# Performance work log

Hardware: AMD Instinct MI355X
Metric: run time of the kernel (lower is better)

Reference implementation:

```python
import jax, jax.numpy as jnp
import numpy as np

N_NODES = 100000
N_EDGES = 3200000
N_GRAPHS = 128
F_IN, HID = 16, 64


def setup_inputs() -> dict:
    key = jax.random.key(0)
    ks = jax.random.split(key, 16)
    def lin(k, fan_in, fan_out):
        bound = 1.0 / np.sqrt(fan_in)
        kw, kb = jax.random.split(k)
        W = jax.random.uniform(kw, (fan_in, fan_out), jnp.float32, -bound, bound)
        b = jax.random.uniform(kb, (fan_out,), jnp.float32, -bound, bound)
        return W, b
    x = jax.random.normal(ks[0], (N_NODES, F_IN), jnp.float32)
    edge_index = jax.random.randint(ks[1], (2, N_EDGES), 0, N_NODES, jnp.int64 if jax.config.jax_enable_x64 else jnp.int32)
    edge_attr = jax.random.normal(ks[2], (N_EDGES, 4), jnp.float32)
    batch = jnp.sort(jax.random.randint(ks[3], (N_NODES,), 0, N_GRAPHS))
    W1, b1 = lin(ks[4], F_IN, HID)
    W2, b2 = lin(ks[5], HID, HID)
    W3, b3 = lin(ks[6], HID, HID)
    Wf1, bf1 = lin(ks[7], HID, 32)
    Wf2, bf2 = lin(ks[8], 32, 1)
    return dict(x=x, edge_index=edge_index, edge_attr=edge_attr, batch=batch,
                W1=W1, b1=b1, W2=W2, b2=b2, W3=W3, b3=b3,
                Wf1=Wf1, bf1=bf1, Wf2=Wf2, bf2=bf2)


def _gcn_conv(x, src, dst, norm, W, b, n_nodes):
    # PyG GCNConv: out = scatter_add(norm * (x @ W)[src] -> dst) + b
    h = x @ W                                   # [N, out]
    msg = h[src] * norm[:, None]                # [E+N, out] gather + scale
    agg = jax.ops.segment_sum(msg, dst, num_segments=n_nodes)
    return agg + b


def reference(x, edge_index, edge_attr, batch, W1, b1, W2, b2, W3, b3, Wf1, bf1, Wf2, bf2):
    n = x.shape[0]
    # add self loops (GCNConv default)
    loop = jnp.arange(n, dtype=edge_index.dtype)
    src = jnp.concatenate([edge_index[0], loop])
    dst = jnp.concatenate([edge_index[1], loop])
    # symmetric degree normalization: deg computed on dst with self loops
    deg = jax.ops.segment_sum(jnp.ones_like(src, dtype=x.dtype), dst, num_segments=n)
    dinv = jax.lax.rsqrt(jnp.maximum(deg, 1.0))
    norm = dinv[src] * dinv[dst]

    h = jax.nn.relu(_gcn_conv(x, src, dst, norm, W1, b1, n))   # dropout = identity (eval)
    h = jax.nn.relu(_gcn_conv(h, src, dst, norm, W2, b2, n))
    h = jax.nn.relu(_gcn_conv(h, src, dst, norm, W3, b3, n))

    # global mean pool over graphs
    sums = jax.ops.segment_sum(h, batch, num_segments=N_GRAPHS)          # [B, HID]
    cnts = jax.ops.segment_sum(jnp.ones((n,), x.dtype), batch, num_segments=N_GRAPHS)
    pooled = sums / jnp.maximum(cnts, 1.0)[:, None]

    z = jax.nn.relu(pooled @ Wf1 + bf1)
    return z @ Wf2 + bf2                                                  # [B, 1]
```

## Files before the change

kernel.cpp:

```cpp
#include <hip/hip_runtime.h>
#include <hip/hip_bf16.h>

#define HID 64
#define MAXNB 2048
#define NBLK 512
#define FILL_T 1024
#define HREP 4

__device__ __forceinline__ float bf2f(unsigned short u) {
    return __uint_as_float(((unsigned)u) << 16);
}
__device__ __forceinline__ unsigned short f2bf(float f) {
    __hip_bfloat16 b = __float2bfloat16(f);
    return *(unsigned short*)&b;
}


__global__ __launch_bounds__(FILL_T) void radix_hist_kernel(
    const int* __restrict__ ei, int* __restrict__ H, int* __restrict__ bhist,
    int E, int NB, int C) {
    __shared__ int lh[HREP * (MAXNB + 1)];
    int blk = blockIdx.x, tid = threadIdx.x;
    for (int i = tid; i < HREP * (MAXNB + 1); i += FILL_T) lh[i] = 0;
    __syncthreads();
    int* lhr = lh + ((tid >> 6) & (HREP - 1)) * (MAXNB + 1);
    int lo = blk * C, hi = min(lo + C, E);
    int cnt = hi - lo;
    int n4 = ((E & 3) == 0) ? (cnt >> 2) : 0;
    const int4* d4 = (const int4*)(ei + (long long)E + lo);
    for (int k = tid; k < n4; k += FILL_T) {
        int4 d = d4[k];
        atomicAdd(&lhr[d.x >> 6], 1);
        atomicAdd(&lhr[d.y >> 6], 1);
        atomicAdd(&lhr[d.z >> 6], 1);
        atomicAdd(&lhr[d.w >> 6], 1);
    }
    for (int e = lo + (n4 << 2) + tid; e < hi; e += FILL_T)
        atomicAdd(&lhr[ei[(long long)E + e] >> 6], 1);
    __syncthreads();
    for (int i = tid; i < NB; i += FILL_T) {
        int v = 0;
#pragma unroll
        for (int r = 0; r < HREP; r++) v += lh[r * (MAXNB + 1) + i];
        H[blk * NB + i] = v;
        if (v) atomicAdd(&bhist[i], v);
    }
}

__global__ __launch_bounds__(256) void scan_kernel(
    const int* __restrict__ bhist, int* __restrict__ pptr, int* __restrict__ gcur, int NB) {
    __shared__ int ssum[256];
    int tid = threadIdx.x;
    int C = (NB + 255) / 256;
    int lo = tid * C, hi = min(lo + C, NB);
    int s = 0;
    for (int i = lo; i < hi; i++) s += bhist[i];
    ssum[tid] = s;
    __syncthreads();
    for (int off = 1; off < 256; off <<= 1) {
        int v = (tid >= off) ? ssum[tid - off] : 0;
        __syncthreads();
        ssum[tid] += v;
        __syncthreads();
    }
    int run = (tid == 0) ? 0 : ssum[tid - 1];
    for (int i = lo; i < hi; i++) {
        pptr[i] = run;
        gcur[i] = run;
        run += bhist[i];
    }
    if (hi == NB) pptr[NB] = run;
}

__global__ __launch_bounds__(FILL_T) void radix_fill_kernel(
    const int* __restrict__ ei, const int* __restrict__ H, int* __restrict__ gcur,
    unsigned* __restrict__ ebuf, int E, int NB, int C) {
    __shared__ int lcur[MAXNB];
    int blk = blockIdx.x, tid = threadIdx.x;
    for (int i = tid; i < NB; i += FILL_T) {
        int c = H[blk * NB + i];
        lcur[i] = c ? atomicAdd(&gcur[i], c) : 0;
    }
    __syncthreads();
    int lo = blk * C, hi = min(lo + C, E);
    int cnt = hi - lo;
    int n4 = ((E & 3) == 0) ? (cnt >> 2) : 0;
    const int4* s4 = (const int4*)(ei + lo);
    const int4* d4 = (const int4*)(ei + (long long)E + lo);
    for (int k = tid; k < n4; k += FILL_T) {
        int4 s = s4[k];
        int4 d = d4[k];
        int p0 = atomicAdd(&lcur[d.x >> 6], 1);
        int p1 = atomicAdd(&lcur[d.y >> 6], 1);
        int p2 = atomicAdd(&lcur[d.z >> 6], 1);
        int p3 = atomicAdd(&lcur[d.w >> 6], 1);
        ebuf[p0] = ((unsigned)s.x << 6) | (unsigned)(d.x & 63);
        ebuf[p1] = ((unsigned)s.y << 6) | (unsigned)(d.y & 63);
        ebuf[p2] = ((unsigned)s.z << 6) | (unsigned)(d.z & 63);
        ebuf[p3] = ((unsigned)s.w << 6) | (unsigned)(d.w & 63);
    }
    for (int e = lo + (n4 << 2) + tid; e < hi; e += FILL_T) {
        int s = ei[e];
        int d = ei[(long long)E + e];
        int pos = atomicAdd(&lcur[d >> 6], 1);
        ebuf[pos] = ((unsigned)s << 6) | (unsigned)(d & 63);
    }
}

__global__ __launch_bounds__(256) void node_csr_kernel(
    const int* __restrict__ pptr, const unsigned* __restrict__ ebuf,
    int* __restrict__ row_ptr, int* __restrict__ col, float* __restrict__ dinv,
    int N, int NB) {
    __shared__ int lcnt[64];
    __shared__ int loff[64];
    __shared__ int lcur[64];
    int bkt = blockIdx.x, tid = threadIdx.x;
    int beg = pptr[bkt], end = pptr[bkt + 1];
    if (tid < 64) lcnt[tid] = 0;
    __syncthreads();
    for (int e = beg + tid; e < end; e += 256) atomicAdd(&lcnt[ebuf[e] & 63u], 1);
    __syncthreads();
    if (tid < 64) {
        int v = lcnt[tid];
        int p = v;
#pragma unroll
        for (int off = 1; off < 64; off <<= 1) {
            int t = __shfl_up(p, off);
            if (tid >= off) p += t;
        }
        int base = beg + p - v;
        loff[tid] = base;
        lcur[tid] = base;
        int node = (bkt << 6) + tid;
        if (node < N) {
            row_ptr[node] = base;
            dinv[node] = rsqrtf((float)(v + 1));
        }
    }
    if (tid == 0 && bkt == NB - 1) row_ptr[N] = pptr[NB];
    __syncthreads();
    for (int e = beg + tid; e < end; e += 256) {
        unsigned ev = ebuf[e];
        int pos = atomicAdd(&lcur[ev & 63u], 1);
        col[pos] = (int)(ev >> 6);
    }
}

template <typename Tin, int K>
__global__ void gemm_g_kernel(const Tin* __restrict__ in,
                              const float* __restrict__ W,
                              const float* __restrict__ dinv,
                              unsigned short* __restrict__ g, int N) {
    __shared__ float sW[K * HID];
    __shared__ float sIn[16 * K];
    int tid = threadIdx.x;
    for (int idx = tid; idx < K * HID; idx += 256) sW[idx] = W[idx];
    int base = blockIdx.x * 16;
    for (int idx = tid; idx < 16 * K; idx += 256) {
        int r = idx / K, c = idx % K;
        int node = base + r;
        float v = 0.f;
        if (node < N) {
            Tin t = in[(long long)node * K + c];
            if constexpr (sizeof(Tin) == 2) v = bf2f((unsigned short)t);
            else v = (float)t;
        }
        sIn[idx] = v;
    }
    __syncthreads();
    int j = tid & 63;
    int si = tid >> 6;
#pragma unroll
    for (int u = 0; u < 4; u++) {
        int r = si * 4 + u;
        int node = base + r;
        if (node >= N) continue;
        float acc = 0.f;
#pragma unroll
        for (int k = 0; k < K; k++) acc += sIn[r * K + k] * sW[k * HID + j];
        g[(long long)node * HID + j] = f2bf(dinv[node] * acc);
    }
}

__global__ __launch_bounds__(256) void gather_kernel(
    const int* __restrict__ row_ptr, const int* __restrict__ col,
    const unsigned short* __restrict__ g, const float* __restrict__ dinv,
    const float* __restrict__ bias, unsigned short* __restrict__ h, int N) {
    int wv = __builtin_amdgcn_readfirstlane(threadIdx.x >> 6);
    int node = blockIdx.x * 4 + wv;
    int lane = threadIdx.x & 63;
    if (node >= N) return;
    int beg = row_ptr[node], end = row_ptr[node + 1];
    float sum = bf2f(g[(long long)node * HID + lane]);
    int j = beg;
    for (; j + 8 <= end; j += 8) {
        int s0 = col[j + 0], s1 = col[j + 1], s2 = col[j + 2], s3 = col[j + 3];
        int s4 = col[j + 4], s5 = col[j + 5], s6 = col[j + 6], s7 = col[j + 7];
        float f0 = bf2f(g[(long long)s0 * HID + lane]);
        float f1 = bf2f(g[(long long)s1 * HID + lane]);
        float f2 = bf2f(g[(long long)s2 * HID + lane]);
        float f3 = bf2f(g[(long long)s3 * HID + lane]);
        float f4 = bf2f(g[(long long)s4 * HID + lane]);
        float f5 = bf2f(g[(long long)s5 * HID + lane]);
        float f6 = bf2f(g[(long long)s6 * HID + lane]);
        float f7 = bf2f(g[(long long)s7 * HID + lane]);
        sum += ((f0 + f1) + (f2 + f3)) + ((f4 + f5) + (f6 + f7));
    }
    for (; j < end; j++) {
        sum += bf2f(g[(long long)col[j] * HID + lane]);
    }
    float v = dinv[node] * sum + bias[lane];
    h[(long long)node * HID + lane] = f2bf(v > 0.f ? v : 0.f);
}

__global__ void pool_kernel(const unsigned short* __restrict__ h, const int* __restrict__ batch,
                            float* __restrict__ sums, float* __restrict__ cnt, int N) {
    int wave = blockIdx.x * 4 + (threadIdx.x >> 6);
    int lane = threadIdx.x & 63;
    int lo = wave * 16;
    if (lo >= N) return;
    int hi = min(lo + 16, N);
    int curb = batch[lo];
    float sum = 0.f;
    int nseg = 0;
    for (int i = lo; i < hi; i++) {
        int b = batch[i];
        if (b != curb) {
            atomicAdd(&sums[curb * HID + lane], sum);
            if (lane == 0) atomicAdd(&cnt[curb], (float)nseg);
            curb = b; sum = 0.f; nseg = 0;
        }
        sum += bf2f(h[(long long)i * HID + lane]);
        nseg++;
    }
    atomicAdd(&sums[curb * HID + lane], sum);
    if (lane == 0) atomicAdd(&cnt[curb], (float)nseg);
}

__global__ void final_kernel(const float* __restrict__ sums, const float* __restrict__ cnt,
                             const float* __restrict__ Wf1, const float* __restrict__ bf1,
                             const float* __restrict__ Wf2, const float* __restrict__ bf2,
                             float* __restrict__ out) {
    __shared__ float sW1[HID * 32];
    __shared__ float sW2[32];
    int tid = threadIdx.x;
    for (int idx = tid; idx < HID * 32; idx += 128) sW1[idx] = Wf1[idx];
    if (tid < 32) sW2[tid] = Wf2[tid];
    __syncthreads();
    int b = tid;
    float pooled[HID];
    float c = fmaxf(cnt[b], 1.0f);
#pragma unroll
    for (int j = 0; j < HID; j++) pooled[j] = sums[b * HID + j] / c;
    float o = bf2[0];
#pragma unroll 4
    for (int hd = 0; hd < 32; hd++) {
        float z = bf1[hd];
#pragma unroll
        for (int j = 0; j < HID; j++) z += pooled[j] * sW1[j * 32 + hd];
        z = fmaxf(z, 0.f);
        o += z * sW2[hd];
    }
    out[b] = o;
}

extern "C" void kernel_launch(void* const* d_in, const int* in_sizes, int n_in,
                              void* d_out, int out_size, void* d_ws, size_t ws_size,
                              hipStream_t stream) {
    const float* x     = (const float*)d_in[0];
    const int*   ei    = (const int*)d_in[1];
    const int*   batch = (const int*)d_in[3];
    const float* W1  = (const float*)d_in[4];
    const float* b1  = (const float*)d_in[5];
    const float* W2  = (const float*)d_in[6];
    const float* b2  = (const float*)d_in[7];
    const float* W3  = (const float*)d_in[8];
    const float* b3  = (const float*)d_in[9];
    const float* Wf1 = (const float*)d_in[10];
    const float* bf1 = (const float*)d_in[11];
    const float* Wf2 = (const float*)d_in[12];
    const float* bf2 = (const float*)d_in[13];
    float* out = (float*)d_out;

    const int N  = in_sizes[0] / 16;
    const int E  = in_sizes[1] / 2;
    const int NB = (N + 63) / 64;

    char* ws = (char*)d_ws;
    size_t o = 0;
    float*          dinv    = (float*)(ws + o);          o += ((size_t)N * 4 + 4095) / 4096 * 4096;
    int*            row_ptr = (int*)(ws + o);            o += ((size_t)(N + 1) * 4 + 4095) / 4096 * 4096;
    int*            pptr    = (int*)(ws + o);            o += ((size_t)(NB + 1) * 4 + 4095) / 4096 * 4096;
    int*            bhist   = (int*)(ws + o);            o += ((size_t)NB * 4 + 4095) / 4096 * 4096;
    int*            gcur    = (int*)(ws + o);            o += ((size_t)NB * 4 + 4095) / 4096 * 4096;
    int*            H       = (int*)(ws + o);            o += ((size_t)NBLK * NB * 4 + 4095) / 4096 * 4096;
    unsigned*       ebuf    = (unsigned*)(ws + o);       o += (size_t)E * 4;
    int*            col     = (int*)(ws + o);            o += (size_t)E * 4;
    unsigned short* A       = (unsigned short*)(ws + o); o += (size_t)N * HID * 2;
    unsigned short* B       = (unsigned short*)(ws + o); o += (size_t)N * HID * 2;
    float*          sums    = (float*)(ws + o);          o += 128 * HID * 4;
    float*          cnt     = (float*)(ws + o);          o += 128 * 4;
    (void)ws_size;

    const int T = 256;
    const int Cchunk = (((E + NBLK - 1) / NBLK) + 3) & ~3;
    const int gGm = (N + 15) / 16;
    const int gGa = (N + 3) / 4;
    const int gPool = ((N + 15) / 16 + 3) / 4;

    hipMemsetAsync(bhist, 0, (size_t)NB * 4, stream);
    radix_hist_kernel<<<NBLK, FILL_T, 0, stream>>>(ei, H, bhist, E, NB, Cchunk);
    scan_kernel<<<1, T, 0, stream>>>(bhist, pptr, gcur, NB);
    radix_fill_kernel<<<NBLK, FILL_T, 0, stream>>>(ei, H, gcur, ebuf, E, NB, Cchunk);
    node_csr_kernel<<<NB, T, 0, stream>>>(pptr, ebuf, row_ptr, col, dinv, N, NB);

    gemm_g_kernel<float, 16><<<gGm, T, 0, stream>>>(x, W1, dinv, A, N);
    gather_kernel<<<gGa, T, 0, stream>>>(row_ptr, col, A, dinv, b1, B, N);

    gemm_g_kernel<unsigned short, 64><<<gGm, T, 0, stream>>>(B, W2, dinv, B, N);
    gather_kernel<<<gGa, T, 0, stream>>>(row_ptr, col, B, dinv, b2, A, N);

    gemm_g_kernel<unsigned short, 64><<<gGm, T, 0, stream>>>(A, W3, dinv, A, N);
    gather_kernel<<<gGa, T, 0, stream>>>(row_ptr, col, A, dinv, b3, B, N);

    hipMemsetAsync(sums, 0, (128 * HID + 128) * 4, stream);
    pool_kernel<<<gPool, T, 0, stream>>>(B, batch, sums, cnt, N);
    final_kernel<<<1, 128, 0, stream>>>(sums, cnt, Wf1, bf1, Wf2, bf2, out);
}
```

Measured before the change: 549.4 us.

## Gather neighbor rows with 16-byte loads, eight edges per wave in parallel

Rewrites the CSR gather so that each wave splits into 8 groups of 8 lanes. Each lane loads 8 bf16 features in one 16-byte load, so a wave fetches 8 neighbor rows per instruction, replacing the old pattern of one 2-byte element per lane per row. Partial sums are combined across groups with xor shuffles, and only 8 lanes write the output row as packed 16-byte stores. The aim is fewer memory instructions and more loads in flight per node. The cost is shuffle reduction overhead and idle lanes on low-degree nodes.

```diff
diff --git a/kernel.cpp b/kernel.cpp
--- a/kernel.cpp
+++ b/kernel.cpp
@@ -182,6 +182,17 @@
     }
 }
 
+__device__ __forceinline__ void add8(float* acc, uint4 r) {
+    acc[0] += __uint_as_float(r.x << 16);
+    acc[1] += __uint_as_float(r.x & 0xffff0000u);
+    acc[2] += __uint_as_float(r.y << 16);
+    acc[3] += __uint_as_float(r.y & 0xffff0000u);
+    acc[4] += __uint_as_float(r.z << 16);
+    acc[5] += __uint_as_float(r.z & 0xffff0000u);
+    acc[6] += __uint_as_float(r.w << 16);
+    acc[7] += __uint_as_float(r.w & 0xffff0000u);
+}
+
 __global__ __launch_bounds__(256) void gather_kernel(
     const int* __restrict__ row_ptr, const int* __restrict__ col,
     const unsigned short* __restrict__ g, const float* __restrict__ dinv,
@@ -190,27 +201,67 @@
     int node = blockIdx.x * 4 + wv;
     int lane = threadIdx.x & 63;
     if (node >= N) return;
+    int grp = lane >> 3;
+    int c = lane & 7;
     int beg = row_ptr[node], end = row_ptr[node + 1];
-    float sum = bf2f(g[(long long)node * HID + lane]);
-    int j = beg;
-    for (; j + 8 <= end; j += 8) {
-        int s0 = col[j + 0], s1 = col[j + 1], s2 = col[j + 2], s3 = col[j + 3];
-        int s4 = col[j + 4], s5 = col[j + 5], s6 = col[j + 6], s7 = col[j + 7];
-        float f0 = bf2f(g[(long long)s0 * HID + lane]);
-        float f1 = bf2f(g[(long long)s1 * HID + lane]);
-        float f2 = bf2f(g[(long long)s2 * HID + lane]);
-        float f3 = bf2f(g[(long long)s3 * HID + lane]);
-        float f4 = bf2f(g[(long long)s4 * HID + lane]);
-        float f5 = bf2f(g[(long long)s5 * HID + lane]);
-        float f6 = bf2f(g[(long long)s6 * HID + lane]);
-        float f7 = bf2f(g[(long long)s7 * HID + lane]);
-        sum += ((f0 + f1) + (f2 + f3)) + ((f4 + f5) + (f6 + f7));
-    }
-    for (; j < end; j++) {
-        sum += bf2f(g[(long long)col[j] * HID + lane]);
-    }
-    float v = dinv[node] * sum + bias[lane];
-    h[(long long)node * HID + lane] = f2bf(v > 0.f ? v : 0.f);
+
+    float acc[8] = {0.f, 0.f, 0.f, 0.f, 0.f, 0.f, 0.f, 0.f};
+    if (grp == 0) {
+        uint4 rs = *(const uint4*)(g + ((long long)node << 6) + (c << 3));
+        add8(acc, rs);
+    }
+
+    for (int base = beg; base < end; base += 32) {
+        int e0 = base + grp;
+        int e1 = e0 + 8, e2 = e0 + 16, e3 = e0 + 24;
+        bool k0 = e0 < end, k1 = e1 < end, k2 = e2 < end, k3 = e3 < end;
+        int c0 = k0 ? col[e0] : 0;
+        int c1 = k1 ? col[e1] : 0;
+        int c2 = k2 ? col[e2] : 0;
+        int c3 = k3 ? col[e3] : 0;
+        uint4 r0 = *(const uint4*)(g + (((long long)c0) << 6) + (c << 3));
+        uint4 r1 = *(const uint4*)(g + (((long long)c1) << 6) + (c << 3));
+        uint4 r2 = *(const uint4*)(g + (((long long)c2) << 6) + (c << 3));
+        uint4 r3 = *(const uint4*)(g + (((long long)c3) << 6) + (c << 3));
+        if (k0) add8(acc, r0);
+        if (k1) add8(acc, r1);
+        if (k2) add8(acc, r2);
+        if (k3) add8(acc, r3);
+    }
+
+#pragma unroll
+    for (int m = 8; m <= 32; m <<= 1) {
+#pragma unroll
+        for (int k = 0; k < 8; k++) acc[k] += __shfl_xor(acc[k], m);
+    }
+
+    if (lane < 8) {
+        float dv = dinv[node];
+        float4 ba = *(const float4*)(bias + (lane << 3));
+        float4 bb = *(const float4*)(bias + (lane << 3) + 4);
+        float v0 = dv * acc[0] + ba.x;
+        float v1 = dv * acc[1] + ba.y;
+        float v2 = dv * acc[2] + ba.z;
+        float v3 = dv * acc[3] + ba.w;
+        float v4 = dv * acc[4] + bb.x;
+        float v5 = dv * acc[5] + bb.y;
+        float v6 = dv * acc[6] + bb.z;
+        float v7 = dv * acc[7] + bb.w;
+        v0 = v0 > 0.f ? v0 : 0.f;
+        v1 = v1 > 0.f ? v1 : 0.f;
+        v2 = v2 > 0.f ? v2 : 0.f;
+        v3 = v3 > 0.f ? v3 : 0.f;
+        v4 = v4 > 0.f ? v4 : 0.f;
+        v5 = v5 > 0.f ? v5 : 0.f;
+        v6 = v6 > 0.f ? v6 : 0.f;
+        v7 = v7 > 0.f ? v7 : 0.f;
+        uint4 w;
+        w.x = (unsigned)f2bf(v0) | ((unsigned)f2bf(v1) << 16);
+        w.y = (unsigned)f2bf(v2) | ((unsigned)f2bf(v3) << 16);
+        w.z = (unsigned)f2bf(v4) | ((unsigned)f2bf(v5) << 16);
+        w.w = (unsigned)f2bf(v6) | ((unsigned)f2bf(v7) << 16);
+        *(uint4*)(h + ((long long)node << 6) + (lane << 3)) = w;
+    }
 }
 
 __global__ void pool_kernel(const unsigned short* __restrict__ h, const int* __restrict__ batch,
```

Result: faster. 522.8 us (-4.8%).
